# Optimization experiments

Measured on AMD Instinct MI355X. Metric: run time of the kernel, lower is better.

## Reference

```python
import jax, jax.numpy as jnp
import numpy as np

B, N, C = 8, 4096, 320
HEAD, SR = 5, 2
HEAD_DIM = C // HEAD
SCALE = HEAD_DIM ** -0.5
LN_EPS = 1e-5


def setup_inputs() -> dict:
    key = jax.random.key(0)
    ks = jax.random.split(key, 8)
    s = 0.02
    return {
        "x": jax.random.normal(ks[0], (B, N, C), jnp.float32),
        "q_w": jax.random.normal(ks[1], (C, C), jnp.float32) * s,
        "q_b": jnp.zeros((C,), jnp.float32),
        "kv_w": jax.random.normal(ks[2], (C, 2 * C), jnp.float32) * s,
        "kv_b": jnp.zeros((2 * C,), jnp.float32),
        "sr_w": jax.random.normal(ks[3], (SR, SR, C, C), jnp.float32) * s,  # HWIO
        "sr_b": jnp.zeros((C,), jnp.float32),
        "ln_g": jnp.ones((C,), jnp.float32),
        "ln_b": jnp.zeros((C,), jnp.float32),
        "proj_w": jax.random.normal(ks[4], (C, C), jnp.float32) * s,
        "proj_b": jnp.zeros((C,), jnp.float32),
        "H": 64,
        "W": 64,
    }


def reference(x, q_w, q_b, kv_w, kv_b, sr_w, sr_b, ln_g, ln_b, proj_w, proj_b, H, W):
    b, n, c = x.shape
    # q projection -> [B, head, N, d]
    q = (x @ q_w + q_b).reshape(b, n, HEAD, HEAD_DIM).transpose(0, 2, 1, 3)
    # spatial reduction of KV: strided conv (kernel=stride=SR) + LayerNorm
    x_img = x.reshape(b, H, W, c)  # NHWC
    x_ = jax.lax.conv_general_dilated(
        x_img, sr_w, window_strides=(SR, SR), padding="VALID",
        dimension_numbers=("NHWC", "HWIO", "NHWC")) + sr_b
    x_ = x_.reshape(b, -1, c)  # [B, N/SR^2, C]
    mu = jnp.mean(x_, axis=-1, keepdims=True)
    var = jnp.mean(jnp.square(x_ - mu), axis=-1, keepdims=True)
    x_ = (x_ - mu) * jax.lax.rsqrt(var + LN_EPS) * ln_g + ln_b
    # kv projection -> k, v each [B, head, Nkv, d]
    kv = (x_ @ kv_w + kv_b).reshape(b, -1, 2, HEAD, HEAD_DIM)
    k = kv[:, :, 0].transpose(0, 2, 1, 3)
    v = kv[:, :, 1].transpose(0, 2, 1, 3)
    # attention
    attn = jnp.einsum("bhnd,bhmd->bhnm", q, k) * SCALE
    attn = jax.nn.softmax(attn, axis=-1)
    out = jnp.einsum("bhnm,bhmd->bhnd", attn, v)
    out = out.transpose(0, 2, 1, 3).reshape(b, n, c)
    return out @ proj_w + proj_b
```

## Files before the change

kernel.cpp:

```cpp
#include <hip/hip_runtime.h>

typedef __attribute__((ext_vector_type(8))) short bf16x8;
typedef __attribute__((ext_vector_type(4))) short bf16x4;
typedef __attribute__((ext_vector_type(4))) float f32x4;
typedef __attribute__((ext_vector_type(2))) float f32x2;
typedef __attribute__((ext_vector_type(2))) unsigned u32x2;
typedef __attribute__((ext_vector_type(4))) unsigned u32x4;

#define DEVI static __device__ __forceinline__
#define AS1 __attribute__((address_space(1)))
#define AS3 __attribute__((address_space(3)))

DEVI unsigned short f2bf(float f) {
  unsigned u = __builtin_bit_cast(unsigned, f);
  return (unsigned short)((u + 0x7FFFu + ((u >> 16) & 1u)) >> 16);
}

DEVI unsigned pkbf(float a, float b) {
#if __has_builtin(__builtin_amdgcn_cvt_pk_bf16_f32)
  return __builtin_bit_cast(unsigned, __builtin_amdgcn_cvt_pk_bf16_f32(a, b));
#else
  return (unsigned)f2bf(a) | ((unsigned)f2bf(b) << 16);
#endif
}

DEVI float fast_exp2(float x) {
#if __has_builtin(__builtin_amdgcn_exp2f)
  return __builtin_amdgcn_exp2f(x);
#else
  return exp2f(x);
#endif
}

DEVI void gl_lds16(const unsigned short* g, unsigned short* l) {
  __builtin_amdgcn_global_load_lds((const AS1 unsigned int*)g, (AS3 unsigned int*)l, 16, 0, 0);
}

DEVI size_t frag_off(int row, int k, int KG) {
  return ((size_t)(row >> 4) * KG + (k >> 3)) * 128 + (row & 15) * 8 + (k & 7);
}

__global__ __launch_bounds__(256)
void k_prep(const float* __restrict__ x, unsigned short* __restrict__ xf) {
  __shared__ __align__(16) unsigned short L[20480];
  const int t = threadIdx.x;
  const size_t base = (size_t)blockIdx.x * 64 * 320;
#pragma unroll
  for (int i = 0; i < 10; i++) {
    int c = i * 256 + t;
    const float* p = x + base + (size_t)c * 8;
    f32x4 a = ((const f32x4*)p)[0], b = ((const f32x4*)p)[1];
    u32x4 pk = {pkbf(a[0], a[1]), pkbf(a[2], a[3]), pkbf(b[0], b[1]), pkbf(b[2], b[3])};
    int r = c / 40, g = c - r * 40;
    int gidx = ((r >> 4) * 40 + g) * 16 + (r & 15);
    int sidx = gidx ^ ((gidx >> 4) & 7);
    *(u32x4*)(L + sidx * 8) = pk;
  }
  __syncthreads();
  unsigned short* outb = xf + base;
#pragma unroll
  for (int i = 0; i < 10; i++) {
    int o = i * 256 + t;
    int sidx = o ^ ((o >> 4) & 7);
    *(u32x4*)(outb + (size_t)o * 8) = *(const u32x4*)(L + sidx * 8);
  }
}

__global__ __launch_bounds__(256)
void k_transpose_all(const float* __restrict__ q_w, const float* __restrict__ kv_w,
                     const float* __restrict__ proj_w, const float* __restrict__ sr_w,
                     unsigned short* __restrict__ Wq, unsigned short* __restrict__ Wkv,
                     unsigned short* __restrict__ Wp, unsigned short* __restrict__ Wsr) {
  const float* src; unsigned short* dst; int K, N;
  switch (blockIdx.z) {
    case 0:  src = q_w;    dst = Wq;  K = 320;  N = 320; break;
    case 1:  src = kv_w;   dst = Wkv; K = 320;  N = 640; break;
    case 2:  src = proj_w; dst = Wp;  K = 320;  N = 320; break;
    default: src = sr_w;   dst = Wsr; K = 1280; N = 320; break;
  }
  if ((int)blockIdx.x >= (K >> 5) || (int)blockIdx.y >= (N >> 5)) return;
  const int KG = K >> 3;
  __shared__ float tile[32][33];
  const int k0 = blockIdx.x * 32, n0 = blockIdx.y * 32;
  const int tx = threadIdx.x, ty = threadIdx.y;
#pragma unroll
  for (int i = 0; i < 4; i++)
    tile[ty + i * 8][tx] = src[(size_t)(k0 + ty + i * 8) * N + n0 + tx];
  __syncthreads();
#pragma unroll
  for (int i = 0; i < 4; i++) {
    int n = n0 + ty + i * 8, k = k0 + tx;
    dst[frag_off(n, k, KG)] = f2bf(tile[tx][ty + i * 8]);
  }
}

__global__ __launch_bounds__(256)
void k_ln(const float* __restrict__ xc, const float* __restrict__ gam,
          const float* __restrict__ bet, unsigned short* __restrict__ xr) {
  const int row = blockIdx.x * 4 + (threadIdx.x >> 6);
  const int l = threadIdx.x & 63;
  const float* p = xc + (size_t)row * 320;
  float s = 0.f, ss = 0.f;
#pragma unroll
  for (int i = 0; i < 5; i++) { float v = p[l + 64 * i]; s += v; ss += v * v; }
#pragma unroll
  for (int o = 1; o < 64; o <<= 1) { s += __shfl_xor(s, o); ss += __shfl_xor(ss, o); }
  float mu = s * (1.f / 320.f);
  float var = ss * (1.f / 320.f) - mu * mu;
  float rstd = rsqrtf(var + 1e-5f);
  if (l < 40) {
    f32x4 a = ((const f32x4*)(p + l * 8))[0], b = ((const f32x4*)(p + l * 8))[1];
    f32x4 ga = ((const f32x4*)(gam + l * 8))[0], gb = ((const f32x4*)(gam + l * 8))[1];
    f32x4 ba = ((const f32x4*)(bet + l * 8))[0], bb = ((const f32x4*)(bet + l * 8))[1];
    f32x4 ya, yb;
#pragma unroll
    for (int j = 0; j < 4; j++) {
      ya[j] = (a[j] - mu) * rstd * ga[j] + ba[j];
      yb[j] = (b[j] - mu) * rstd * gb[j] + bb[j];
    }
    u32x4 pk = {pkbf(ya[0], ya[1]), pkbf(ya[2], ya[3]), pkbf(yb[0], yb[1]), pkbf(yb[2], yb[3])};
    *(u32x4*)(xr + ((size_t)((row >> 4) * 40 + l)) * 128 + (row & 15) * 8) = pk;
  }
}

template <int MT, int AK, int EPI, int NSEG>
__global__ __launch_bounds__(256)
void k_gemm(const unsigned short* __restrict__ A, const unsigned short* __restrict__ W,
            const float* __restrict__ bias, void* __restrict__ outp, void* __restrict__ outp2,
            float oscale) {
  __shared__ __align__(16) unsigned short Bl[20480];
  const int t = threadIdx.x, w = t >> 6, ln = t & 63, lr = ln & 15, lq = ln >> 4;
  const int m0 = blockIdx.x * (MT * 64), n0 = blockIdx.y * 64;

  f32x4 acc[MT][4];
#pragma unroll
  for (int i = 0; i < MT; i++)
#pragma unroll
    for (int j = 0; j < 4; j++) acc[i][j] = (f32x4){0.f, 0.f, 0.f, 0.f};

  int crt[MT], crow[MT];
  if (AK == 1) {
#pragma unroll
    for (int mi = 0; mi < MT; mi++) {
      int gm = m0 + (w * MT + mi) * 16;
      int b = gm >> 10, p = gm & 1023, oy = p >> 5, ox0 = p & 31;
      crt[mi] = b * 256 + ((2 * oy) * 64 + 2 * ox0) >> 4;
      crow[mi] = 0;
      (void)crow[mi];
    }
  }

#pragma unroll
  for (int seg = 0; seg < NSEG; seg++) {
    const int kh = seg >> 1, kw = seg & 1;
    if (seg) __syncthreads();
    if (AK == 0) {
      const unsigned short* Ws = W + ((size_t)(n0 >> 4) * 40) * 128;
#pragma unroll
      for (int j = 0; j < 10; j++)
        gl_lds16(Ws + (size_t)(j * 4 + w) * 512 + ln * 8, Bl + (j * 4 + w) * 512);
    } else {
      const unsigned short* Wt = W + ((size_t)((n0 >> 4) + w) * 160 + seg * 40) * 128;
#pragma unroll
      for (int j = 0; j < 10; j++)
        gl_lds16(Wt + (size_t)j * 512 + ln * 8, Bl + w * 5120 + j * 512);
    }
    __syncthreads();

#pragma unroll
    for (int ks = 0; ks < 10; ks++) {
      bf16x8 af[MT], bfr[4];
#pragma unroll
      for (int mi = 0; mi < MT; mi++) {
        if (AK == 0) {
          af[mi] = *(const bf16x8*)(
              A + ((size_t)((m0 >> 4) + w * MT + mi) * 40 + ks * 4 + lq) * 128 + lr * 8);
        } else {
          int gm = m0 + (w * MT + mi) * 16;
          int b = gm >> 10, p = gm & 1023, oy = p >> 5, ox0 = p & 31;
          int r0 = (2 * oy + kh) * 64 + 2 * ox0 + kw;
          int brt = b * 256 + (r0 >> 4);
          af[mi] = *(const bf16x8*)(
              A + ((size_t)(brt + (lr >> 3)) * 40 + ks * 4 + lq) * 128 +
              (kw + 2 * (lr & 7)) * 8);
        }
      }
#pragma unroll
      for (int ni = 0; ni < 4; ni++)
        bfr[ni] = *(const bf16x8*)(Bl + ((ni * 40) + ks * 4 + lq) * 128 + lr * 8);
#pragma unroll
      for (int mi = 0; mi < MT; mi++)
#pragma unroll
        for (int ni = 0; ni < 4; ni++)
          acc[mi][ni] =
              __builtin_amdgcn_mfma_f32_16x16x32_bf16(af[mi], bfr[ni], acc[mi][ni], 0, 0, 0);
    }
  }

  if (EPI == 0) {
    unsigned short* out = (unsigned short*)outp;
    const int h = n0 >> 6;
#pragma unroll
    for (int mi = 0; mi < MT; mi++)
#pragma unroll
      for (int ni = 0; ni < 4; ni++)
#pragma unroll
        for (int rr = 0; rr < 4; rr++) {
          int gm = m0 + (w * MT + mi) * 16 + lq * 4 + rr;
          int b = gm >> 12, n = gm & 4095, d = ni * 16 + lr;
          out[((size_t)(b * 5 + h) << 18) + ((size_t)n << 6) + d] =
              f2bf((acc[mi][ni][rr] + bias[n0 + d]) * oscale);
        }
  } else if (EPI == 3) {
    float* out = (float*)outp;
#pragma unroll
    for (int mi = 0; mi < MT; mi++)
#pragma unroll
      for (int ni = 0; ni < 4; ni++)
#pragma unroll
        for (int rr = 0; rr < 4; rr++) {
          int gm = m0 + (w * MT + mi) * 16 + lq * 4 + rr;
          int gc = n0 + ni * 16 + lr;
          out[(size_t)gm * 320 + gc] = acc[mi][ni][rr] + bias[gc];
        }
  } else {
    if (n0 < 320) {
      unsigned short* out = (unsigned short*)outp;
      const int h = n0 >> 6;
#pragma unroll
      for (int mi = 0; mi < MT; mi++)
#pragma unroll
        for (int ni = 0; ni < 4; ni++)
#pragma unroll
          for (int rr = 0; rr < 4; rr++) {
            int gm = m0 + (w * MT + mi) * 16 + lq * 4 + rr;
            int b = gm >> 10, mm = gm & 1023, d = ni * 16 + lr;
            out[((size_t)(b * 5 + h) << 16) + ((size_t)mm << 6) + d] =
                f2bf(acc[mi][ni][rr] + bias[n0 + d]);
          }
    } else {
      unsigned short* out = (unsigned short*)outp2;
      const int h = (n0 - 320) >> 6;
      unsigned short* Tl = (unsigned short*)Bl;
      __syncthreads();
#pragma unroll
      for (int mi = 0; mi < MT; mi++)
#pragma unroll
        for (int ni = 0; ni < 4; ni++)
#pragma unroll
          for (int rr = 0; rr < 4; rr++) {
            int ml = (w * MT + mi) * 16 + lq * 4 + rr;
            int d = ni * 16 + lr;
            Tl[d * 136 + ml] = f2bf(acc[mi][ni][rr] + bias[n0 + d]);
          }
      __syncthreads();
      const int b = m0 >> 10, mm0 = m0 & 1023;
#pragma unroll
      for (int i = 0; i < 4; i++) {
        int ch = t + 256 * i, d = ch >> 4, g = ch & 15;
        *(bf16x8*)(out + ((size_t)(b * 5 + h) << 16) + d * 1024 + mm0 + g * 8) =
            *(const bf16x8*)(Tl + d * 136 + g * 8);
      }
    }
  }
}

__global__ __launch_bounds__(256)
void k_attn(const unsigned short* __restrict__ Qb, const unsigned short* __restrict__ Kb,
            const unsigned short* __restrict__ Vt, unsigned short* __restrict__ AO) {
  __shared__ __align__(16) unsigned char smem[32768];
  const int t = threadIdx.x, w = t >> 6, ln = t & 63, lr = ln & 15, lq = ln >> 4;
  const int bh = blockIdx.y;
  const int m0 = blockIdx.x * 128 + w * 32;
  const unsigned short* Qp = Qb + ((size_t)bh << 18);
  const unsigned short* Kp = Kb + ((size_t)bh << 16);
  const unsigned short* Vp = Vt + ((size_t)bh << 16);

  bf16x8 qf[2][2];
#pragma unroll
  for (int mt = 0; mt < 2; mt++)
#pragma unroll
    for (int t2 = 0; t2 < 2; t2++)
      qf[mt][t2] = *(const bf16x8*)(Qp + (size_t)(m0 + mt * 16 + lr) * 64 + t2 * 32 + lq * 8);

  f32x4 oacc[4][2];
  f32x2 den2[2] = {(f32x2){0.f, 0.f}, (f32x2){0.f, 0.f}};
#pragma unroll
  for (int dt = 0; dt < 4; dt++)
#pragma unroll
    for (int mt = 0; mt < 2; mt++) oacc[dt][mt] = (f32x4){0.f, 0.f, 0.f, 0.f};

  const int rS = ln >> 3, sS = ln & 7;

  auto stage = [&](int c, int buf) {
    unsigned short* KL = (unsigned short*)(smem + buf * 16384);
    unsigned short* VL = KL + 4096;
#pragma unroll
    for (int i = 0; i < 2; i++) {
      int r = (w * 2 + i) * 8 + rS;
      int g = sS ^ (r & 7);
      gl_lds16(Kp + (size_t)(c * 64 + r) * 64 + g * 8, KL + (w * 2 + i) * 512);
      gl_lds16(Vp + (size_t)r * 1024 + c * 64 + g * 8, VL + (w * 2 + i) * 512);
    }
  };

  stage(0, 0);
  __syncthreads();

  for (int c = 0; c < 16; c++) {
    if (c < 15) stage(c + 1, (c + 1) & 1);
    const unsigned short* KL = (const unsigned short*)(smem + (c & 1) * 16384);
    const unsigned short* VL = KL + 4096;

    f32x4 sacc[4][2];
#pragma unroll
    for (int kt = 0; kt < 4; kt++) {
      int kr = 16 * kt + lr;
      bf16x8 kf0 = *(const bf16x8*)(KL + kr * 64 + ((lq ^ (lr & 7)) * 8));
      bf16x8 kf1 = *(const bf16x8*)(KL + kr * 64 + (((4 + lq) ^ (lr & 7)) * 8));
#pragma unroll
      for (int mt = 0; mt < 2; mt++) {
        f32x4 s = (f32x4){0.f, 0.f, 0.f, 0.f};
        s = __builtin_amdgcn_mfma_f32_16x16x32_bf16(kf0, qf[mt][0], s, 0, 0, 0);
        s = __builtin_amdgcn_mfma_f32_16x16x32_bf16(kf1, qf[mt][1], s, 0, 0, 0);
        sacc[kt][mt] = s;
      }
    }

#pragma unroll
    for (int tp = 0; tp < 2; tp++) {
      bf16x8 pf8[2];
#pragma unroll
      for (int mt = 0; mt < 2; mt++) {
        f32x4 ea, eb;
#pragma unroll
        for (int j = 0; j < 4; j++) {
          ea[j] = fast_exp2(sacc[2 * tp][mt][j]);
          eb[j] = fast_exp2(sacc[2 * tp + 1][mt][j]);
        }
        den2[mt] += (f32x2){ea[0], ea[1]} + (f32x2){ea[2], ea[3]};
        den2[mt] += (f32x2){eb[0], eb[1]} + (f32x2){eb[2], eb[3]};
        u32x4 pk = {pkbf(ea[0], ea[1]), pkbf(ea[2], ea[3]),
                    pkbf(eb[0], eb[1]), pkbf(eb[2], eb[3])};
        pf8[mt] = __builtin_bit_cast(bf16x8, pk);
      }
#pragma unroll
      for (int dt = 0; dt < 4; dt++) {
        int vr = dt * 16 + lr;
        const unsigned short* vbase = VL + vr * 64;
        int ga = 4 * tp + (lq >> 1), gb = ga + 2;
        bf16x4 vlo = *(const bf16x4*)(vbase + (ga ^ (lr & 7)) * 8 + (lq & 1) * 4);
        bf16x4 vhi = *(const bf16x4*)(vbase + (gb ^ (lr & 7)) * 8 + (lq & 1) * 4);
        bf16x8 vf8 = {vlo[0], vlo[1], vlo[2], vlo[3], vhi[0], vhi[1], vhi[2], vhi[3]};
#pragma unroll
        for (int mt = 0; mt < 2; mt++)
          oacc[dt][mt] =
              __builtin_amdgcn_mfma_f32_16x16x32_bf16(vf8, pf8[mt], oacc[dt][mt], 0, 0, 0);
      }
    }
    __syncthreads();
  }

  float inv[2];
#pragma unroll
  for (int mt = 0; mt < 2; mt++) {
    float s = den2[mt][0] + den2[mt][1];
    s += __shfl_xor(s, 16);
    s += __shfl_xor(s, 32);
    inv[mt] = 1.f / s;
  }

  const int b = bh / 5, h = bh - b * 5;
  const int rt0 = b * 256 + (m0 >> 4);
#pragma unroll
  for (int mt = 0; mt < 2; mt++)
#pragma unroll
    for (int dt = 0; dt < 4; dt++) {
      float i0 = inv[mt];
      u32x2 pk = {pkbf(oacc[dt][mt][0] * i0, oacc[dt][mt][1] * i0),
                  pkbf(oacc[dt][mt][2] * i0, oacc[dt][mt][3] * i0)};
      int colg = h * 8 + dt * 2 + (lq >> 1);
      size_t off = ((size_t)(rt0 + mt) * 40 + colg) * 128 + lr * 8 + (lq & 1) * 4;
      *(u32x2*)(AO + off) = pk;
    }
}

extern "C" void kernel_launch(void* const* d_in, const int* in_sizes, int n_in,
                              void* d_out, int out_size, void* d_ws, size_t ws_size,
                              hipStream_t stream) {
  (void)in_sizes; (void)n_in; (void)out_size; (void)ws_size;
  const float* x      = (const float*)d_in[0];
  const float* q_w    = (const float*)d_in[1];
  const float* q_b    = (const float*)d_in[2];
  const float* kv_w   = (const float*)d_in[3];
  const float* kv_b   = (const float*)d_in[4];
  const float* sr_w   = (const float*)d_in[5];
  const float* sr_b   = (const float*)d_in[6];
  const float* ln_g   = (const float*)d_in[7];
  const float* ln_b   = (const float*)d_in[8];
  const float* proj_w = (const float*)d_in[9];
  const float* proj_b = (const float*)d_in[10];
  float* out = (float*)d_out;

  char* ws = (char*)d_ws;
  size_t off = 0;
  auto alloc = [&](size_t bytes) {
    void* p = ws + off;
    off += (bytes + 255) & ~(size_t)255;
    return p;
  };
  unsigned short* xbf_fr = (unsigned short*)alloc((size_t)32768 * 320 * 2);
  unsigned short* Qb     = (unsigned short*)alloc((size_t)32768 * 320 * 2);
  unsigned short* KbP    = (unsigned short*)alloc((size_t)40 * 65536 * 2);
  unsigned short* VtP    = (unsigned short*)alloc((size_t)40 * 65536 * 2);
  float*          xc     = (float*)alloc((size_t)8192 * 320 * 4);
  unsigned short* xr     = (unsigned short*)alloc((size_t)8192 * 320 * 2);
  unsigned short* Wq_fr  = (unsigned short*)alloc((size_t)320 * 320 * 2);
  unsigned short* Wkv_fr = (unsigned short*)alloc((size_t)640 * 320 * 2);
  unsigned short* Wp_fr  = (unsigned short*)alloc((size_t)320 * 320 * 2);
  unsigned short* Wsr_fr = (unsigned short*)alloc((size_t)320 * 1280 * 2);
  unsigned short* AO = xbf_fr;

  const float S2 = 0.125f * 1.4426950408889634f;

  k_prep<<<512, 256, 0, stream>>>(x, xbf_fr);
  k_transpose_all<<<dim3(40, 20, 4), dim3(32, 8), 0, stream>>>(
      q_w, kv_w, proj_w, sr_w, Wq_fr, Wkv_fr, Wp_fr, Wsr_fr);

  k_gemm<2, 1, 3, 4><<<dim3(64, 5), 256, 0, stream>>>(xbf_fr, Wsr_fr, sr_b, xc, nullptr, 1.f);
  k_ln<<<2048, 256, 0, stream>>>(xc, ln_g, ln_b, xr);
  k_gemm<4, 0, 0, 1><<<dim3(128, 5), 256, 0, stream>>>(xbf_fr, Wq_fr, q_b, Qb, nullptr, S2);
  k_gemm<2, 0, 4, 1><<<dim3(64, 10), 256, 0, stream>>>(xr, Wkv_fr, kv_b, KbP, VtP, 1.f);
  k_attn<<<dim3(32, 40), 256, 0, stream>>>(Qb, KbP, VtP, AO);
  k_gemm<4, 0, 3, 1><<<dim3(128, 5), 256, 0, stream>>>(AO, Wp_fr, proj_b, out, nullptr, 1.f);
}
```

Baseline: 233.1 us.

## Merge pack kernels, enlarge attention blocks, shrink GEMM M-tiles

Fuses the x-to-bf16 conversion and the four weight transposes into one launch, which removes a kernel launch. The attention kernel now uses 512-thread blocks covering 256 query rows, so each K/V chunk staged in shared memory is reused by twice as many waves and each thread issues fewer staging loads. The Q and output-projection GEMMs drop from 4 to 2 M-subtiles per wave with twice as many blocks, trading per-block reuse for more parallelism. Unused conv index code is removed.

```diff
diff --git a/kernel.cpp b/kernel.cpp
--- a/kernel.cpp
+++ b/kernel.cpp
@@ -41,56 +41,56 @@
 }
 
 __global__ __launch_bounds__(256)
-void k_prep(const float* __restrict__ x, unsigned short* __restrict__ xf) {
-  __shared__ __align__(16) unsigned short L[20480];
-  const int t = threadIdx.x;
-  const size_t base = (size_t)blockIdx.x * 64 * 320;
-#pragma unroll
-  for (int i = 0; i < 10; i++) {
-    int c = i * 256 + t;
-    const float* p = x + base + (size_t)c * 8;
-    f32x4 a = ((const f32x4*)p)[0], b = ((const f32x4*)p)[1];
-    u32x4 pk = {pkbf(a[0], a[1]), pkbf(a[2], a[3]), pkbf(b[0], b[1]), pkbf(b[2], b[3])};
-    int r = c / 40, g = c - r * 40;
-    int gidx = ((r >> 4) * 40 + g) * 16 + (r & 15);
-    int sidx = gidx ^ ((gidx >> 4) & 7);
-    *(u32x4*)(L + sidx * 8) = pk;
-  }
-  __syncthreads();
-  unsigned short* outb = xf + base;
-#pragma unroll
-  for (int i = 0; i < 10; i++) {
-    int o = i * 256 + t;
-    int sidx = o ^ ((o >> 4) & 7);
-    *(u32x4*)(outb + (size_t)o * 8) = *(const u32x4*)(L + sidx * 8);
-  }
-}
-
-__global__ __launch_bounds__(256)
-void k_transpose_all(const float* __restrict__ q_w, const float* __restrict__ kv_w,
-                     const float* __restrict__ proj_w, const float* __restrict__ sr_w,
-                     unsigned short* __restrict__ Wq, unsigned short* __restrict__ Wkv,
-                     unsigned short* __restrict__ Wp, unsigned short* __restrict__ Wsr) {
-  const float* src; unsigned short* dst; int K, N;
-  switch (blockIdx.z) {
-    case 0:  src = q_w;    dst = Wq;  K = 320;  N = 320; break;
-    case 1:  src = kv_w;   dst = Wkv; K = 320;  N = 640; break;
-    case 2:  src = proj_w; dst = Wp;  K = 320;  N = 320; break;
-    default: src = sr_w;   dst = Wsr; K = 1280; N = 320; break;
-  }
-  if ((int)blockIdx.x >= (K >> 5) || (int)blockIdx.y >= (N >> 5)) return;
-  const int KG = K >> 3;
-  __shared__ float tile[32][33];
-  const int k0 = blockIdx.x * 32, n0 = blockIdx.y * 32;
-  const int tx = threadIdx.x, ty = threadIdx.y;
-#pragma unroll
-  for (int i = 0; i < 4; i++)
-    tile[ty + i * 8][tx] = src[(size_t)(k0 + ty + i * 8) * N + n0 + tx];
-  __syncthreads();
-#pragma unroll
-  for (int i = 0; i < 4; i++) {
-    int n = n0 + ty + i * 8, k = k0 + tx;
-    dst[frag_off(n, k, KG)] = f2bf(tile[tx][ty + i * 8]);
+void k_pack(const float* __restrict__ x, const float* __restrict__ q_w,
+            const float* __restrict__ kv_w, const float* __restrict__ proj_w,
+            const float* __restrict__ sr_w, unsigned short* __restrict__ xf,
+            unsigned short* __restrict__ Wq, unsigned short* __restrict__ Wkv,
+            unsigned short* __restrict__ Wp, unsigned short* __restrict__ Wsr) {
+  __shared__ __align__(16) unsigned char smem[40960];
+  const int bid = blockIdx.x;
+  if (bid < 512) {
+    unsigned short* L = (unsigned short*)smem;
+    const int t = threadIdx.y * 32 + threadIdx.x;
+    const size_t base = (size_t)bid * 64 * 320;
+#pragma unroll
+    for (int i = 0; i < 10; i++) {
+      int c = i * 256 + t;
+      const float* p = x + base + (size_t)c * 8;
+      f32x4 a = ((const f32x4*)p)[0], b = ((const f32x4*)p)[1];
+      u32x4 pk = {pkbf(a[0], a[1]), pkbf(a[2], a[3]), pkbf(b[0], b[1]), pkbf(b[2], b[3])};
+      int r = c / 40, g = c - r * 40;
+      int gidx = ((r >> 4) * 40 + g) * 16 + (r & 15);
+      int sidx = gidx ^ ((gidx >> 4) & 7);
+      *(u32x4*)(L + sidx * 8) = pk;
+    }
+    __syncthreads();
+    unsigned short* outb = xf + base;
+#pragma unroll
+    for (int i = 0; i < 10; i++) {
+      int o = i * 256 + t;
+      int sidx = o ^ ((o >> 4) & 7);
+      *(u32x4*)(outb + (size_t)o * 8) = *(const u32x4*)(L + sidx * 8);
+    }
+  } else {
+    int e = bid - 512;
+    const float* src; unsigned short* dst; int K, N, kt, nt;
+    if (e < 100)      { src = q_w;    dst = Wq;  K = 320;  N = 320; kt = e / 10;  nt = e - kt * 10; }
+    else if (e < 300) { int i = e - 100; src = kv_w; dst = Wkv; K = 320; N = 640; kt = i / 20; nt = i - kt * 20; }
+    else if (e < 400) { int i = e - 300; src = proj_w; dst = Wp; K = 320; N = 320; kt = i / 10; nt = i - kt * 10; }
+    else              { int i = e - 400; src = sr_w; dst = Wsr; K = 1280; N = 320; kt = i / 10; nt = i - kt * 10; }
+    const int KG = K >> 3;
+    float (*tile)[33] = (float(*)[33])smem;
+    const int k0 = kt * 32, n0 = nt * 32;
+    const int tx = threadIdx.x, ty = threadIdx.y;
+#pragma unroll
+    for (int i = 0; i < 4; i++)
+      tile[ty + i * 8][tx] = src[(size_t)(k0 + ty + i * 8) * N + n0 + tx];
+    __syncthreads();
+#pragma unroll
+    for (int i = 0; i < 4; i++) {
+      int n = n0 + ty + i * 8, k = k0 + tx;
+      dst[frag_off(n, k, KG)] = f2bf(tile[tx][ty + i * 8]);
+    }
   }
 }
 
@@ -137,18 +137,6 @@
   for (int i = 0; i < MT; i++)
 #pragma unroll
     for (int j = 0; j < 4; j++) acc[i][j] = (f32x4){0.f, 0.f, 0.f, 0.f};
-
-  int crt[MT], crow[MT];
-  if (AK == 1) {
-#pragma unroll
-    for (int mi = 0; mi < MT; mi++) {
-      int gm = m0 + (w * MT + mi) * 16;
-      int b = gm >> 10, p = gm & 1023, oy = p >> 5, ox0 = p & 31;
-      crt[mi] = b * 256 + ((2 * oy) * 64 + 2 * ox0) >> 4;
-      crow[mi] = 0;
-      (void)crow[mi];
-    }
-  }
 
 #pragma unroll
   for (int seg = 0; seg < NSEG; seg++) {
@@ -241,7 +229,7 @@
     } else {
       unsigned short* out = (unsigned short*)outp2;
       const int h = (n0 - 320) >> 6;
-      unsigned short* Tl = (unsigned short*)Bl;
+      unsigned short* Tl = Bl;
       __syncthreads();
 #pragma unroll
       for (int mi = 0; mi < MT; mi++)
@@ -265,13 +253,13 @@
   }
 }
 
-__global__ __launch_bounds__(256)
+__global__ __launch_bounds__(512)
 void k_attn(const unsigned short* __restrict__ Qb, const unsigned short* __restrict__ Kb,
             const unsigned short* __restrict__ Vt, unsigned short* __restrict__ AO) {
   __shared__ __align__(16) unsigned char smem[32768];
   const int t = threadIdx.x, w = t >> 6, ln = t & 63, lr = ln & 15, lq = ln >> 4;
   const int bh = blockIdx.y;
-  const int m0 = blockIdx.x * 128 + w * 32;
+  const int m0 = blockIdx.x * 256 + w * 32;
   const unsigned short* Qp = Qb + ((size_t)bh << 18);
   const unsigned short* Kp = Kb + ((size_t)bh << 16);
   const unsigned short* Vp = Vt + ((size_t)bh << 16);
@@ -295,13 +283,10 @@
   auto stage = [&](int c, int buf) {
     unsigned short* KL = (unsigned short*)(smem + buf * 16384);
     unsigned short* VL = KL + 4096;
-#pragma unroll
-    for (int i = 0; i < 2; i++) {
-      int r = (w * 2 + i) * 8 + rS;
-      int g = sS ^ (r & 7);
-      gl_lds16(Kp + (size_t)(c * 64 + r) * 64 + g * 8, KL + (w * 2 + i) * 512);
-      gl_lds16(Vp + (size_t)r * 1024 + c * 64 + g * 8, VL + (w * 2 + i) * 512);
-    }
+    int r = w * 8 + rS;
+    int g = sS ^ (r & 7);
+    gl_lds16(Kp + (size_t)(c * 64 + r) * 64 + g * 8, KL + w * 512);
+    gl_lds16(Vp + (size_t)r * 1024 + c * 64 + g * 8, VL + w * 512);
   };
 
   stage(0, 0);
@@ -423,14 +408,13 @@
 
   const float S2 = 0.125f * 1.4426950408889634f;
 
-  k_prep<<<512, 256, 0, stream>>>(x, xbf_fr);
-  k_transpose_all<<<dim3(40, 20, 4), dim3(32, 8), 0, stream>>>(
-      q_w, kv_w, proj_w, sr_w, Wq_fr, Wkv_fr, Wp_fr, Wsr_fr);
+  k_pack<<<1312, dim3(32, 8), 0, stream>>>(x, q_w, kv_w, proj_w, sr_w,
+                                           xbf_fr, Wq_fr, Wkv_fr, Wp_fr, Wsr_fr);
 
   k_gemm<2, 1, 3, 4><<<dim3(64, 5), 256, 0, stream>>>(xbf_fr, Wsr_fr, sr_b, xc, nullptr, 1.f);
   k_ln<<<2048, 256, 0, stream>>>(xc, ln_g, ln_b, xr);
-  k_gemm<4, 0, 0, 1><<<dim3(128, 5), 256, 0, stream>>>(xbf_fr, Wq_fr, q_b, Qb, nullptr, S2);
+  k_gemm<2, 0, 0, 1><<<dim3(256, 5), 256, 0, stream>>>(xbf_fr, Wq_fr, q_b, Qb, nullptr, S2);
   k_gemm<2, 0, 4, 1><<<dim3(64, 10), 256, 0, stream>>>(xr, Wkv_fr, kv_b, KbP, VtP, 1.f);
-  k_attn<<<dim3(32, 40), 256, 0, stream>>>(Qb, KbP, VtP, AO);
-  k_gemm<4, 0, 3, 1><<<dim3(128, 5), 256, 0, stream>>>(AO, Wp_fr, proj_b, out, nullptr, 1.f);
-}
+  k_attn<<<dim3(16, 40), 512, 0, stream>>>(Qb, KbP, VtP, AO);
+  k_gemm<2, 0, 3, 1><<<dim3(256, 5), 256, 0, stream>>>(AO, Wp_fr, proj_b, out, nullptr, 1.f);
+}
```

Result: slower. 240.7 us (+3.3%).
